# Optimization experiments

Measured on AMD Instinct MI355X. Metric: run time of the kernel, lower is better.

## Reference

```python
import jax, jax.numpy as jnp
import numpy as np

B, TQ, TK, DK, DV = 64, 1024, 1024, 64, 64


def setup_inputs() -> dict:
    key = jax.random.key(0)
    kq, kk, kv, km = jax.random.split(key, 4)
    q = jax.random.normal(kq, (B, TQ, DK), dtype=jnp.float32)
    k = jax.random.normal(kk, (B, TK, DK), dtype=jnp.float32)
    v = jax.random.normal(kv, (B, TK, DV), dtype=jnp.float32)
    mask = jax.random.randint(km, (B, TQ, TK), 0, 2).astype(jnp.int32)
    return {"q": q, "k": k, "v": v, "mask": mask}


def reference(q, k, v, mask):
    # attn = q @ k^T / sqrt(d_k)   -> [B, TQ, TK]
    temper = jnp.sqrt(jnp.asarray(q.shape[-1], dtype=jnp.float32))
    attn = jnp.einsum('bqd,bkd->bqk', q, k) / temper
    # mask-add: -1e9 where mask == 0
    mmask = -1e9 * (1.0 - mask.astype(jnp.float32))
    attn = attn + mmask
    attn = jax.nn.softmax(attn, axis=-1)
    # dropout rate is 0.0 -> identity
    out = jnp.einsum('bqk,bkd->bqd', attn, v)
    return (out, attn)
```

## Files before the change

kernel.cpp:

```cpp
#include <hip/hip_runtime.h>
#include <hip/hip_bf16.h>


#define B_   64
#define TQ_  1024
#define TK_  1024
#define DD   64

typedef short short8 __attribute__((ext_vector_type(8)));
typedef float f32x4 __attribute__((ext_vector_type(4)));

#define PLW    68
#define PL_U32 (16 * PLW)
#define VSTR   40
#define VT_SH  (64 * VSTR)
#define WVS    (2 * PL_U32 + VT_SH)

__device__ __forceinline__ unsigned cvt2(float a, float b) {
    __hip_bfloat162 h = __float22bfloat162_rn(make_float2(a, b));
    unsigned u; __builtin_memcpy(&u, &h, 4); return u;
}

union Frag { short8 s; unsigned u[4]; };

__global__ __launch_bounds__(256, 4) void attn_mfma_kernel(
    const float* __restrict__ qg, const float* __restrict__ kg,
    const float* __restrict__ vg, const int* __restrict__ maskg,
    float* __restrict__ outg, float* __restrict__ attng)
{
    __shared__ __align__(16) short lds[4 * WVS];
    __shared__ float red[128];

    const int t    = threadIdx.x;
    const int wave = t >> 6, lane = t & 63;
    const int quad = lane >> 4, n16 = lane & 15;
    const int b    = blockIdx.y;
    const int q0   = blockIdx.x * 16;
    const int kbase = wave * 256;

    short*    wbase = lds + wave * WVS;
    unsigned* pl    = (unsigned*)wbase;
    short*    vw    = wbase + 2 * PL_U32;

    Frag aq[2];
    {
        const float* qp = qg + ((size_t)(b * TQ_ + q0 + n16)) * DD + quad * 8;
        #pragma unroll
        for (int f = 0; f < 2; ++f) {
            float4 x = *(const float4*)(qp + f * 32);
            float4 y = *(const float4*)(qp + f * 32 + 4);
            aq[f].u[0] = cvt2(0.125f * x.x, 0.125f * x.y);
            aq[f].u[1] = cvt2(0.125f * x.z, 0.125f * x.w);
            aq[f].u[2] = cvt2(0.125f * y.x, 0.125f * y.y);
            aq[f].u[3] = cvt2(0.125f * y.z, 0.125f * y.w);
        }
    }

    float s_reg[64];

    const float* kbp  = kg + (size_t)b * TK_ * DD;
    const int*   mrow = maskg + ((size_t)(b * TQ_ + q0 + n16)) * TK_ + kbase + quad * 4;
    #pragma unroll
    for (int kt = 0; kt < 16; ++kt) {
        const float* kp = kbp + (size_t)(kbase + kt * 16 + n16) * DD + quad * 8;
        Frag bk[2];
        #pragma unroll
        for (int f = 0; f < 2; ++f) {
            float4 x = *(const float4*)(kp + f * 32);
            float4 y = *(const float4*)(kp + f * 32 + 4);
            bk[f].u[0] = cvt2(x.x, x.y); bk[f].u[1] = cvt2(x.z, x.w);
            bk[f].u[2] = cvt2(y.x, y.y); bk[f].u[3] = cvt2(y.z, y.w);
        }
        const int4 mk = *(const int4*)(mrow + kt * 16);
        f32x4 acc = {0.f, 0.f, 0.f, 0.f};
        acc = __builtin_amdgcn_mfma_f32_16x16x32_bf16(bk[0].s, aq[0].s, acc, 0, 0, 0);
        acc = __builtin_amdgcn_mfma_f32_16x16x32_bf16(bk[1].s, aq[1].s, acc, 0, 0, 0);
        s_reg[kt * 4 + 0] = acc[0] + (mk.x ? 0.f : -1e9f);
        s_reg[kt * 4 + 1] = acc[1] + (mk.y ? 0.f : -1e9f);
        s_reg[kt * 4 + 2] = acc[2] + (mk.z ? 0.f : -1e9f);
        s_reg[kt * 4 + 3] = acc[3] + (mk.w ? 0.f : -1e9f);
    }

    const float* vbp = vg + (size_t)b * TK_ * DD;
    unsigned va16[16];
    #pragma unroll
    for (int i = 0; i < 16; ++i) {
        const float v0 = vbp[(size_t)(kbase + 2 * i) * DD + lane];
        const float v1 = vbp[(size_t)(kbase + 2 * i + 1) * DD + lane];
        va16[i] = cvt2(v0, v1);
    }

    float m8[8];
    #pragma unroll
    for (int j = 0; j < 8; ++j) m8[j] = s_reg[j];
    #pragma unroll
    for (int i = 8; i < 64; i += 8)
        #pragma unroll
        for (int j = 0; j < 8; ++j) m8[j] = fmaxf(m8[j], s_reg[i + j]);
    float m = fmaxf(fmaxf(fmaxf(m8[0], m8[1]), fmaxf(m8[2], m8[3])),
                    fmaxf(fmaxf(m8[4], m8[5]), fmaxf(m8[6], m8[7])));
    m = fmaxf(m, __shfl_xor(m, 16));
    m = fmaxf(m, __shfl_xor(m, 32));
    if (lane < 16) red[wave * 16 + n16] = m;
    __syncthreads();
    const float gm = fmaxf(fmaxf(red[n16], red[16 + n16]),
                           fmaxf(red[32 + n16], red[48 + n16]));
    float l0 = 0.f, l1 = 0.f, l2 = 0.f, l3 = 0.f;
    #pragma unroll
    for (int i = 0; i < 16; ++i) {
        const float p0 = __expf(s_reg[4*i+0] - gm);
        const float p1 = __expf(s_reg[4*i+1] - gm);
        const float p2 = __expf(s_reg[4*i+2] - gm);
        const float p3 = __expf(s_reg[4*i+3] - gm);
        s_reg[4*i+0] = p0; s_reg[4*i+1] = p1;
        s_reg[4*i+2] = p2; s_reg[4*i+3] = p3;
        l0 += p0; l1 += p1; l2 += p2; l3 += p3;
    }
    float lsum = (l0 + l1) + (l2 + l3);
    lsum += __shfl_xor(lsum, 16);
    lsum += __shfl_xor(lsum, 32);
    if (lane < 16) red[64 + wave * 16 + n16] = lsum;
    __syncthreads();
    const float inv = 1.f / (red[64 + n16] + red[80 + n16] +
                             red[96 + n16] + red[112 + n16]);
    #pragma unroll
    for (int i = 0; i < 64; ++i) s_reg[i] *= inv;

    float* ab = attng + ((size_t)(b * TQ_ + q0 + n16)) * TK_ + kbase + quad * 4;
    #pragma unroll
    for (int kt = 0; kt < 16; ++kt)
        *(float4*)(ab + kt * 16) = make_float4(s_reg[kt*4+0], s_reg[kt*4+1],
                                               s_reg[kt*4+2], s_reg[kt*4+3]);
    #pragma unroll
    for (int kt = 0; kt < 8; ++kt) {
        uint2 u;
        u.x = cvt2(s_reg[kt*4+0], s_reg[kt*4+1]);
        u.y = cvt2(s_reg[kt*4+2], s_reg[kt*4+3]);
        *(uint2*)&pl[n16 * PLW + kt * 8 + quad * 2] = u;
    }

    f32x4 oacc[4];
    #pragma unroll
    for (int dg = 0; dg < 4; ++dg) oacc[dg] = (f32x4){0.f, 0.f, 0.f, 0.f};

    #pragma unroll 1
    for (int c = 0; c < 4; ++c) {
        #pragma unroll
        for (int i = 0; i < 16; ++i)
            *(unsigned*)(vw + lane * VSTR + 2 * i) = va16[i];
        {
            const int ck = kbase + (c + 1) * 32;
            #pragma unroll
            for (int i = 0; i < 16; ++i) {
                const float v0 = vbp[(size_t)(ck + 2 * i) * DD + lane];
                const float v1 = vbp[(size_t)(ck + 2 * i + 1) * DD + lane];
                va16[i] = cvt2(v0, v1);
            }
        }
        Frag pf;
        pf.s = *(const short8*)&pl[n16 * PLW + c * 16 + quad * 4];
        #pragma unroll
        for (int dg = 0; dg < 4; ++dg) {
            Frag vf;
            vf.s = *(const short8*)(vw + (dg * 16 + n16) * VSTR + quad * 8);
            oacc[dg] = __builtin_amdgcn_mfma_f32_16x16x32_bf16(vf.s, pf.s, oacc[dg], 0, 0, 0);
        }
    }

    #pragma unroll
    for (int kt = 8; kt < 16; ++kt) {
        uint2 u;
        u.x = cvt2(s_reg[kt*4+0], s_reg[kt*4+1]);
        u.y = cvt2(s_reg[kt*4+2], s_reg[kt*4+3]);
        *(uint2*)&pl[n16 * PLW + (kt - 8) * 8 + quad * 2] = u;
    }

    #pragma unroll 1
    for (int c = 0; c < 4; ++c) {
        #pragma unroll
        for (int i = 0; i < 16; ++i)
            *(unsigned*)(vw + lane * VSTR + 2 * i) = va16[i];
        if (c < 3) {
            const int ck = kbase + (c + 5) * 32;
            #pragma unroll
            for (int i = 0; i < 16; ++i) {
                const float v0 = vbp[(size_t)(ck + 2 * i) * DD + lane];
                const float v1 = vbp[(size_t)(ck + 2 * i + 1) * DD + lane];
                va16[i] = cvt2(v0, v1);
            }
        }
        Frag pf;
        pf.s = *(const short8*)&pl[n16 * PLW + c * 16 + quad * 4];
        #pragma unroll
        for (int dg = 0; dg < 4; ++dg) {
            Frag vf;
            vf.s = *(const short8*)(vw + (dg * 16 + n16) * VSTR + quad * 8);
            oacc[dg] = __builtin_amdgcn_mfma_f32_16x16x32_bf16(vf.s, pf.s, oacc[dg], 0, 0, 0);
        }
    }

    float* ow = (float*)pl;
    #pragma unroll
    for (int dg = 0; dg < 4; ++dg)
        *(f32x4*)&ow[n16 * PLW + dg * 16 + quad * 4] = oacc[dg];
    __syncthreads();
    {
        const int row = t >> 4, col = (t & 15) * 4;
        const float* base = (const float*)lds;
        float4 o = make_float4(0.f, 0.f, 0.f, 0.f);
        #pragma unroll
        for (int w = 0; w < 4; ++w) {
            const float4 x = *(const float4*)(base + w * (WVS / 2) + row * PLW + col);
            o.x += x.x; o.y += x.y; o.z += x.z; o.w += x.w;
        }
        *(float4*)(outg + ((size_t)(b * TQ_ + q0 + row)) * DD + col) = o;
    }
}

extern "C" void kernel_launch(void* const* d_in, const int* in_sizes, int n_in,
                              void* d_out, int out_size, void* d_ws, size_t ws_size,
                              hipStream_t stream) {
    const float* q    = (const float*)d_in[0];
    const float* k    = (const float*)d_in[1];
    const float* v    = (const float*)d_in[2];
    const int*   mask = (const int*)d_in[3];

    float* out  = (float*)d_out;
    float* attn = out + (size_t)B_ * TQ_ * DD;

    dim3 grid(TQ_ / 16, B_);
    attn_mfma_kernel<<<grid, 256, 0, stream>>>(q, k, v, mask, out, attn);
}
```

Before: 653.5 us.

## Load V directly into MFMA fragments, swizzle blocks across XCDs, batch mask loads

V is now read from global memory straight into the MFMA operand layout: each lane loads strided raw floats and converts them in registers, which removes the per-chunk LDS staging of V and its extra reads. The whole P tile is written to LDS once with a wider stride. The PV loop is fully unrolled with the next chunk prefetched. Block indices are remapped so each XCD handles a contiguous group of batches, aiming at better L2 reuse of K and V. Mask int4 loads are issued eight at a time, and launch bounds drop to 3 waves to allow more registers, which may lower occupancy.

```diff
diff --git a/kernel.cpp b/kernel.cpp
--- a/kernel.cpp
+++ b/kernel.cpp
@@ -10,11 +10,8 @@
 typedef short short8 __attribute__((ext_vector_type(8)));
 typedef float f32x4 __attribute__((ext_vector_type(4)));
 
-#define PLW    68
-#define PL_U32 (16 * PLW)
-#define VSTR   40
-#define VT_SH  (64 * VSTR)
-#define WVS    (2 * PL_U32 + VT_SH)
+#define PSTR 264
+#define WVS  (16 * PSTR)
 
 __device__ __forceinline__ unsigned cvt2(float a, float b) {
     __hip_bfloat162 h = __float22bfloat162_rn(make_float2(a, b));
@@ -23,7 +20,7 @@
 
 union Frag { short8 s; unsigned u[4]; };
 
-__global__ __launch_bounds__(256, 4) void attn_mfma_kernel(
+__global__ __launch_bounds__(256, 3) void attn_mfma_kernel(
     const float* __restrict__ qg, const float* __restrict__ kg,
     const float* __restrict__ vg, const int* __restrict__ maskg,
     float* __restrict__ outg, float* __restrict__ attng)
@@ -34,13 +31,14 @@
     const int t    = threadIdx.x;
     const int wave = t >> 6, lane = t & 63;
     const int quad = lane >> 4, n16 = lane & 15;
-    const int b    = blockIdx.y;
-    const int q0   = blockIdx.x * 16;
+
+    const int flat = blockIdx.y * 64 + blockIdx.x;
+    const int xcd  = flat & 7, slot = flat >> 3;
+    const int b    = (xcd << 3) | (slot & 7);
+    const int q0   = (slot >> 3) << 4;
     const int kbase = wave * 256;
 
-    short*    wbase = lds + wave * WVS;
-    unsigned* pl    = (unsigned*)wbase;
-    short*    vw    = wbase + 2 * PL_U32;
+    short* pw = lds + wave * WVS;
 
     Frag aq[2];
     {
@@ -61,34 +59,39 @@
     const float* kbp  = kg + (size_t)b * TK_ * DD;
     const int*   mrow = maskg + ((size_t)(b * TQ_ + q0 + n16)) * TK_ + kbase + quad * 4;
     #pragma unroll
-    for (int kt = 0; kt < 16; ++kt) {
-        const float* kp = kbp + (size_t)(kbase + kt * 16 + n16) * DD + quad * 8;
-        Frag bk[2];
-        #pragma unroll
-        for (int f = 0; f < 2; ++f) {
-            float4 x = *(const float4*)(kp + f * 32);
-            float4 y = *(const float4*)(kp + f * 32 + 4);
-            bk[f].u[0] = cvt2(x.x, x.y); bk[f].u[1] = cvt2(x.z, x.w);
-            bk[f].u[2] = cvt2(y.x, y.y); bk[f].u[3] = cvt2(y.z, y.w);
-        }
-        const int4 mk = *(const int4*)(mrow + kt * 16);
-        f32x4 acc = {0.f, 0.f, 0.f, 0.f};
-        acc = __builtin_amdgcn_mfma_f32_16x16x32_bf16(bk[0].s, aq[0].s, acc, 0, 0, 0);
-        acc = __builtin_amdgcn_mfma_f32_16x16x32_bf16(bk[1].s, aq[1].s, acc, 0, 0, 0);
-        s_reg[kt * 4 + 0] = acc[0] + (mk.x ? 0.f : -1e9f);
-        s_reg[kt * 4 + 1] = acc[1] + (mk.y ? 0.f : -1e9f);
-        s_reg[kt * 4 + 2] = acc[2] + (mk.z ? 0.f : -1e9f);
-        s_reg[kt * 4 + 3] = acc[3] + (mk.w ? 0.f : -1e9f);
-    }
-
-    const float* vbp = vg + (size_t)b * TK_ * DD;
-    unsigned va16[16];
-    #pragma unroll
-    for (int i = 0; i < 16; ++i) {
-        const float v0 = vbp[(size_t)(kbase + 2 * i) * DD + lane];
-        const float v1 = vbp[(size_t)(kbase + 2 * i + 1) * DD + lane];
-        va16[i] = cvt2(v0, v1);
-    }
+    for (int h = 0; h < 2; ++h) {
+        int4 mk[8];
+        #pragma unroll
+        for (int i = 0; i < 8; ++i)
+            mk[i] = *(const int4*)(mrow + (h * 8 + i) * 16);
+        #pragma unroll
+        for (int i = 0; i < 8; ++i) {
+            const int kt = h * 8 + i;
+            const float* kp = kbp + (size_t)(kbase + kt * 16 + n16) * DD + quad * 8;
+            Frag bk[2];
+            #pragma unroll
+            for (int f = 0; f < 2; ++f) {
+                float4 x = *(const float4*)(kp + f * 32);
+                float4 y = *(const float4*)(kp + f * 32 + 4);
+                bk[f].u[0] = cvt2(x.x, x.y); bk[f].u[1] = cvt2(x.z, x.w);
+                bk[f].u[2] = cvt2(y.x, y.y); bk[f].u[3] = cvt2(y.z, y.w);
+            }
+            f32x4 acc = {0.f, 0.f, 0.f, 0.f};
+            acc = __builtin_amdgcn_mfma_f32_16x16x32_bf16(bk[0].s, aq[0].s, acc, 0, 0, 0);
+            acc = __builtin_amdgcn_mfma_f32_16x16x32_bf16(bk[1].s, aq[1].s, acc, 0, 0, 0);
+            s_reg[kt * 4 + 0] = acc[0] + (mk[i].x ? 0.f : -1e9f);
+            s_reg[kt * 4 + 1] = acc[1] + (mk[i].y ? 0.f : -1e9f);
+            s_reg[kt * 4 + 2] = acc[2] + (mk[i].z ? 0.f : -1e9f);
+            s_reg[kt * 4 + 3] = acc[3] + (mk[i].w ? 0.f : -1e9f);
+        }
+    }
+
+    const float* vb0 = vg + (size_t)b * TK_ * DD
+                     + (size_t)(kbase + quad * 8) * DD + n16;
+    float vraw[32];
+    #pragma unroll
+    for (int u = 0; u < 32; ++u)
+        vraw[u] = vb0[(size_t)(u & 7) * DD + (u >> 3) * 16];
 
     float m8[8];
     #pragma unroll
@@ -132,77 +135,45 @@
         *(float4*)(ab + kt * 16) = make_float4(s_reg[kt*4+0], s_reg[kt*4+1],
                                                s_reg[kt*4+2], s_reg[kt*4+3]);
     #pragma unroll
-    for (int kt = 0; kt < 8; ++kt) {
+    for (int kt = 0; kt < 16; ++kt) {
         uint2 u;
         u.x = cvt2(s_reg[kt*4+0], s_reg[kt*4+1]);
         u.y = cvt2(s_reg[kt*4+2], s_reg[kt*4+3]);
-        *(uint2*)&pl[n16 * PLW + kt * 8 + quad * 2] = u;
+        *(uint2*)(pw + n16 * PSTR + kt * 16 + quad * 4) = u;
     }
 
     f32x4 oacc[4];
     #pragma unroll
     for (int dg = 0; dg < 4; ++dg) oacc[dg] = (f32x4){0.f, 0.f, 0.f, 0.f};
 
-    #pragma unroll 1
-    for (int c = 0; c < 4; ++c) {
-        #pragma unroll
-        for (int i = 0; i < 16; ++i)
-            *(unsigned*)(vw + lane * VSTR + 2 * i) = va16[i];
-        {
-            const int ck = kbase + (c + 1) * 32;
+    #pragma unroll
+    for (int c = 0; c < 8; ++c) {
+        unsigned va16[16];
+        #pragma unroll
+        for (int dg = 0; dg < 4; ++dg)
             #pragma unroll
-            for (int i = 0; i < 16; ++i) {
-                const float v0 = vbp[(size_t)(ck + 2 * i) * DD + lane];
-                const float v1 = vbp[(size_t)(ck + 2 * i + 1) * DD + lane];
-                va16[i] = cvt2(v0, v1);
-            }
+            for (int w = 0; w < 4; ++w)
+                va16[dg * 4 + w] = cvt2(vraw[dg * 8 + 2 * w], vraw[dg * 8 + 2 * w + 1]);
+        if (c < 7) {
+            #pragma unroll
+            for (int u = 0; u < 32; ++u)
+                vraw[u] = vb0[(size_t)((c + 1) * 32 + (u & 7)) * DD + (u >> 3) * 16];
         }
         Frag pf;
-        pf.s = *(const short8*)&pl[n16 * PLW + c * 16 + quad * 4];
+        pf.s = *(const short8*)(pw + n16 * PSTR + c * 32 + quad * 8);
         #pragma unroll
         for (int dg = 0; dg < 4; ++dg) {
-            Frag vf;
-            vf.s = *(const short8*)(vw + (dg * 16 + n16) * VSTR + quad * 8);
-            oacc[dg] = __builtin_amdgcn_mfma_f32_16x16x32_bf16(vf.s, pf.s, oacc[dg], 0, 0, 0);
-        }
-    }
-
-    #pragma unroll
-    for (int kt = 8; kt < 16; ++kt) {
-        uint2 u;
-        u.x = cvt2(s_reg[kt*4+0], s_reg[kt*4+1]);
-        u.y = cvt2(s_reg[kt*4+2], s_reg[kt*4+3]);
-        *(uint2*)&pl[n16 * PLW + (kt - 8) * 8 + quad * 2] = u;
-    }
-
-    #pragma unroll 1
-    for (int c = 0; c < 4; ++c) {
-        #pragma unroll
-        for (int i = 0; i < 16; ++i)
-            *(unsigned*)(vw + lane * VSTR + 2 * i) = va16[i];
-        if (c < 3) {
-            const int ck = kbase + (c + 5) * 32;
-            #pragma unroll
-            for (int i = 0; i < 16; ++i) {
-                const float v0 = vbp[(size_t)(ck + 2 * i) * DD + lane];
-                const float v1 = vbp[(size_t)(ck + 2 * i + 1) * DD + lane];
-                va16[i] = cvt2(v0, v1);
-            }
-        }
-        Frag pf;
-        pf.s = *(const short8*)&pl[n16 * PLW + c * 16 + quad * 4];
-        #pragma unroll
-        for (int dg = 0; dg < 4; ++dg) {
-            Frag vf;
-            vf.s = *(const short8*)(vw + (dg * 16 + n16) * VSTR + quad * 8);
-            oacc[dg] = __builtin_amdgcn_mfma_f32_16x16x32_bf16(vf.s, pf.s, oacc[dg], 0, 0, 0);
-        }
-    }
-
-    float* ow = (float*)pl;
+            Frag af;
+            af.u[0] = va16[dg*4+0]; af.u[1] = va16[dg*4+1];
+            af.u[2] = va16[dg*4+2]; af.u[3] = va16[dg*4+3];
+            oacc[dg] = __builtin_amdgcn_mfma_f32_16x16x32_bf16(af.s, pf.s, oacc[dg], 0, 0, 0);
+        }
+    }
+
+    float* ow = (float*)pw;
     #pragma unroll
     for (int dg = 0; dg < 4; ++dg)
-        *(f32x4*)&ow[n16 * PLW + dg * 16 + quad * 4] = oacc[dg];
+        *(f32x4*)&ow[n16 * 68 + dg * 16 + quad * 4] = oacc[dg];
     __syncthreads();
     {
         const int row = t >> 4, col = (t & 15) * 4;
@@ -210,7 +181,7 @@
         float4 o = make_float4(0.f, 0.f, 0.f, 0.f);
         #pragma unroll
         for (int w = 0; w < 4; ++w) {
-            const float4 x = *(const float4*)(base + w * (WVS / 2) + row * PLW + col);
+            const float4 x = *(const float4*)(base + w * (WVS / 2) + row * 68 + col);
             o.x += x.x; o.y += x.y; o.z += x.z; o.w += x.w;
         }
         *(float4*)(outg + ((size_t)(b * TQ_ + q0 + row)) * DD + col) = o;
```

Result: no change. 646.0 us (-1.2%).
